# Kernel optimization log

Hardware: AMD Instinct MI355X
Metric: run time of the kernel (lower is better)

## Reference

```python
import jax, jax.numpy as jnp
import numpy as np

V, Tb, D, H, L = 50257, 1024, 768, 12, 12
HS = D // H  # head size 64
DF = 4 * D   # MLP hidden 3072


def setup_inputs() -> dict:
    key = jax.random.key(0)
    ks = jax.random.split(key, 24)
    s = 0.02
    inp = {}
    inp['x'] = jax.random.randint(ks[0], (1, Tb), 0, V, dtype=jnp.int64)
    inp['wte'] = jax.random.normal(ks[1], (V, D), jnp.float32) * s
    inp['wpe'] = jax.random.normal(ks[2], (Tb, D), jnp.float32) * s
    # per-layer, per-head QKV linears, stacked: [L, H, D, HS]
    inp['Wq'] = jax.random.normal(ks[3], (L, H, D, HS), jnp.float32) * s
    inp['bq'] = jnp.zeros((L, H, HS), jnp.float32)
    inp['Wk'] = jax.random.normal(ks[4], (L, H, D, HS), jnp.float32) * s
    inp['bk'] = jnp.zeros((L, H, HS), jnp.float32)
    inp['Wv'] = jax.random.normal(ks[5], (L, H, D, HS), jnp.float32) * s
    inp['bv'] = jnp.zeros((L, H, HS), jnp.float32)
    inp['ln1_s'] = jnp.ones((L, D), jnp.float32)
    inp['ln1_b'] = jnp.zeros((L, D), jnp.float32)
    inp['W1'] = jax.random.normal(ks[6], (L, D, DF), jnp.float32) * s
    inp['b1'] = jnp.zeros((L, DF), jnp.float32)
    inp['W2'] = jax.random.normal(ks[7], (L, DF, D), jnp.float32) * s
    inp['b2'] = jnp.zeros((L, D), jnp.float32)
    inp['ln2_s'] = jnp.ones((L, D), jnp.float32)
    inp['ln2_b'] = jnp.zeros((L, D), jnp.float32)
    inp['lnf_s'] = jnp.ones((D,), jnp.float32)
    inp['lnf_b'] = jnp.zeros((D,), jnp.float32)
    inp['Wlm'] = jax.random.normal(ks[8], (D, V), jnp.float32) * s
    return inp


def _layernorm(x, scale, bias, eps=1e-5):
    mu = jnp.mean(x, axis=-1, keepdims=True)
    var = jnp.var(x, axis=-1, keepdims=True)
    return (x - mu) * jax.lax.rsqrt(var + eps) * scale + bias


def _gpt2_forward(x, wte, wpe, Wq, bq, Wk, bk, Wv, bv, ln1_s, ln1_b,
                  W1, b1, W2, b2, ln2_s, ln2_b, lnf_s, lnf_b, Wlm):
    B, T = x.shape
    h = wte[x] + wpe[jnp.arange(T)][None]  # [B, T, D]
    mask = jnp.tril(jnp.ones((T, T), jnp.bool_))
    for l in range(L):
        xn = _layernorm(h, ln1_s[l], ln1_b[l])
        # per-head linears, stacked -> [B, H, T, HS]
        q = jnp.einsum('btd,hde->bhte', xn, Wq[l]) + bq[l][None, :, None, :]
        k = jnp.einsum('btd,hde->bhte', xn, Wk[l]) + bk[l][None, :, None, :]
        v = jnp.einsum('btd,hde->bhte', xn, Wv[l]) + bv[l][None, :, None, :]
        # NOTE: original module does NOT scale scores by 1/sqrt(head_size)
        scores = jnp.einsum('bhte,bhse->bhts', q, k)
        scores = jnp.where(mask[None, None], scores, -jnp.inf)
        w = jax.nn.softmax(scores, axis=-1)
        attn = jnp.einsum('bhts,bhse->bhte', w, v)
        attn = attn.transpose(0, 2, 1, 3).reshape(B, T, H * HS)
        h = h + attn  # residual (no output projection in original)
        xn2 = _layernorm(h, ln2_s[l], ln2_b[l])
        mlp = jnp.einsum('btd,df->btf', xn2, W1[l]) + b1[l]
        mlp = jax.nn.gelu(mlp, approximate=False)  # nn.GELU default = exact
        mlp = jnp.einsum('btf,fd->btd', mlp, W2[l]) + b2[l]
        h = h + mlp
    h = _layernorm(h, lnf_s, lnf_b)
    logits = jnp.einsum('btd,dv->btv', h, Wlm)  # lm_head, no bias
    return logits


def reference(x, wte, wpe, Wq, bq, Wk, bk, Wv, bv, ln1_s, ln1_b,
              W1, b1, W2, b2, ln2_s, ln2_b, lnf_s, lnf_b, Wlm):
    return _gpt2_forward(x, wte, wpe, Wq, bq, Wk, bk, Wv, bv, ln1_s, ln1_b,
                         W1, b1, W2, b2, ln2_s, ln2_b, lnf_s, lnf_b, Wlm)
```

## Files before the change

### kernel.cpp

```cpp
#include <hip/hip_runtime.h>
#include <math.h>

#define TLEN 1024
#define DM   768
#define NH   12
#define HSZ  64
#define DF_  3072
#define NL   12
#define VC   50257
#define VCP  50304
#define NPAN (VCP/128)

typedef __attribute__((ext_vector_type(8))) short bf16x8;
typedef __attribute__((ext_vector_type(4))) float f32x4;

__device__ __forceinline__ float gelu_exact(float x){
  return 0.5f * x * (1.0f + erff(x * 0.70710678118654752f));
}
__device__ __forceinline__ short f2bf(float f){
  union { float f; unsigned u; } x; x.f = f;
  unsigned r = x.u + 0x7fffu + ((x.u >> 16) & 1u);
  return (short)(r >> 16);
}
__device__ __forceinline__ void gl16(const void* g, void* l){
  __builtin_amdgcn_global_load_lds(
      (const __attribute__((address_space(1))) unsigned int*)g,
      (__attribute__((address_space(3))) unsigned int*)l, 16, 0, 0);
}

__global__ __launch_bounds__(256) void embedln_k(const int* __restrict__ x,
    const float* __restrict__ wte, const float* __restrict__ wpe,
    const float* __restrict__ sc, const float* __restrict__ bi,
    float* __restrict__ h, short* __restrict__ out)
{
  int w = threadIdx.x >> 6, lane = threadIdx.x & 63;
  int t = blockIdx.x * 4 + w;
  int tok = x[t];
  size_t off = (size_t)t * DM;
  float v[12];
  float s = 0.f, s2 = 0.f;
  #pragma unroll
  for (int i = 0; i < 12; i++){
    int c = lane + i * 64;
    float xv = wte[(size_t)tok * DM + c] + wpe[off + c];
    h[off + c] = xv;
    v[i] = xv; s += xv; s2 += xv * xv;
  }
  #pragma unroll
  for (int o = 32; o; o >>= 1){ s += __shfl_xor(s, o); s2 += __shfl_xor(s2, o); }
  float mu = s * (1.0f / DM);
  float var = s2 * (1.0f / DM) - mu * mu;
  float rs = rsqrtf(var + 1e-5f);
  #pragma unroll
  for (int i = 0; i < 12; i++){
    int c = lane + i * 64;
    out[off + c] = f2bf((v[i] - mu) * rs * sc[c] + bi[c]);
  }
}

__global__ __launch_bounds__(256) void ln_k(const float* __restrict__ in,
    const float* __restrict__ sc, const float* __restrict__ bi,
    short* __restrict__ out)
{
  int w = threadIdx.x >> 6, lane = threadIdx.x & 63;
  int row = blockIdx.x * 4 + w;
  const float* r = in + (size_t)row * DM;
  float v[12];
  float s = 0.f, s2 = 0.f;
  #pragma unroll
  for (int i = 0; i < 12; i++){
    float xv = r[lane + i * 64];
    v[i] = xv; s += xv; s2 += xv * xv;
  }
  #pragma unroll
  for (int o = 32; o; o >>= 1){ s += __shfl_xor(s, o); s2 += __shfl_xor(s2, o); }
  float mu  = s * (1.0f / DM);
  float var = s2 * (1.0f / DM) - mu * mu;
  float rs  = rsqrtf(var + 1e-5f);
  short* o = out + (size_t)row * DM;
  #pragma unroll
  for (int i = 0; i < 12; i++){
    int c = lane + i * 64;
    o[c] = f2bf((v[i] - mu) * rs * sc[c] + bi[c]);
  }
}

__global__ __launch_bounds__(256) void redln_k(float* __restrict__ h,
    const float* __restrict__ p0, const float* __restrict__ p1,
    const float* __restrict__ bias,
    const float* __restrict__ sc, const float* __restrict__ bi,
    short* __restrict__ out)
{
  int w = threadIdx.x >> 6, lane = threadIdx.x & 63;
  int row = blockIdx.x * 4 + w;
  size_t off = (size_t)row * DM;
  float v[12];
  float s = 0.f, s2 = 0.f;
  #pragma unroll
  for (int i = 0; i < 12; i++){
    int c = lane + i * 64;
    float xv = h[off + c] + p0[off + c] + p1[off + c] + bias[c];
    h[off + c] = xv;
    v[i] = xv; s += xv; s2 += xv * xv;
  }
  #pragma unroll
  for (int o = 32; o; o >>= 1){ s += __shfl_xor(s, o); s2 += __shfl_xor(s2, o); }
  float mu  = s * (1.0f / DM);
  float var = s2 * (1.0f / DM) - mu * mu;
  float rs  = rsqrtf(var + 1e-5f);
  #pragma unroll
  for (int i = 0; i < 12; i++){
    int c = lane + i * 64;
    out[off + c] = f2bf((v[i] - mu) * rs * sc[c] + bi[c]);
  }
}

__global__ __launch_bounds__(256) void tc_k(const float* __restrict__ in,
    short* __restrict__ out, int K, int N, int ntiles, int per_mat,
    size_t in_stride, size_t out_stride)
{
  __shared__ short sh[64][65];
  int b = blockIdx.x;
  int l = b / per_mat, r = b - l * per_mat;
  int nt = r % ntiles, kt = r / ntiles;
  const float* ip = in + (size_t)l * in_stride;
  short* op = out + (size_t)l * out_stride;
  int n0 = nt * 64, k0 = kt * 64;
  int tid = threadIdx.x;
  if ((N & 3) == 0){
    #pragma unroll
    for (int it = 0; it < 4; it++){
      int idx = it * 256 + tid;
      int k = idx >> 4, n4 = (idx & 15) * 4;
      float4 v = *(const float4*)(ip + (size_t)(k0 + k) * N + n0 + n4);
      sh[k][n4+0] = f2bf(v.x); sh[k][n4+1] = f2bf(v.y);
      sh[k][n4+2] = f2bf(v.z); sh[k][n4+3] = f2bf(v.w);
    }
  } else {
    #pragma unroll
    for (int it = 0; it < 16; it++){
      int idx = it * 256 + tid;
      int k = idx >> 6, n = idx & 63;
      float v = (n0 + n < N) ? ip[(size_t)(k0 + k) * N + n0 + n] : 0.f;
      sh[k][n] = f2bf(v);
    }
  }
  __syncthreads();
  #pragma unroll
  for (int it = 0; it < 2; it++){
    int n = it * 32 + (tid >> 3);
    int kc = (tid & 7) * 8;
    bf16x8 v;
    #pragma unroll
    for (int u = 0; u < 8; u++) v[u] = sh[kc + u][n];
    *(bf16x8*)(op + (size_t)(n0 + n) * K + k0 + kc) = v;
  }
}

__global__ __launch_bounds__(256) void tcqkv_k(const float* __restrict__ Wq,
    const float* __restrict__ Wk, const float* __restrict__ Wv,
    short* __restrict__ out)
{
  __shared__ short sh[64][65];
  int b = blockIdx.x;
  int l = b / 144; int r = b - l * 144;
  int h = r / 12, kt = r - h * 12;
  int tid = threadIdx.x;
  for (int p = 0; p < 3; p++){
    const float* ip = (p == 0 ? Wq : p == 1 ? Wk : Wv)
                      + ((size_t)(l * NH + h) * DM + kt * 64) * 64;
    if (p) __syncthreads();
    #pragma unroll
    for (int it = 0; it < 4; it++){
      int idx = it * 256 + tid;
      int k = idx >> 4, e4 = (idx & 15) * 4;
      float4 v = *(const float4*)(ip + (size_t)k * 64 + e4);
      sh[k][e4+0] = f2bf(v.x); sh[k][e4+1] = f2bf(v.y);
      sh[k][e4+2] = f2bf(v.z); sh[k][e4+3] = f2bf(v.w);
    }
    __syncthreads();
    short* op = out + (size_t)l * 2304 * DM + (size_t)(p * DM + h * 64) * DM;
    #pragma unroll
    for (int it = 0; it < 2; it++){
      int e = it * 32 + (tid >> 3);
      int kc = (tid & 7) * 8;
      bf16x8 v;
      #pragma unroll
      for (int u = 0; u < 8; u++) v[u] = sh[kc + u][e];
      *(bf16x8*)(op + (size_t)e * DM + kt * 64 + kc) = v;
    }
  }
}

template<int MODE, int FI, int FJ, int BK>
__global__ __launch_bounds__(256) void mg_k(
    const short* __restrict__ A, const short* __restrict__ Bt,
    const float* __restrict__ b0, const float* __restrict__ b1,
    const float* __restrict__ b2,
    void* __restrict__ C0, void* __restrict__ C1, void* __restrict__ C2)
{
  constexpr int LDA    = (MODE == 2) ? DF_ : DM;
  constexpr int BM     = FI * 32;
  constexpr int BN     = FJ * 32;
  constexpr int ABYTES = BM * BK * 2;
  constexpr int BBYTES = BN * BK * 2;
  constexpr int TBYTES = ABYTES + BBYTES;
  constexpr int DEPTH  = 2;
  constexpr int NBUF   = DEPTH + 1;
  constexpr int GR     = BK / 8;
  constexpr int NCHA   = ABYTES / 4096;
  constexpr int NCHB   = BBYTES / 4096;
  constexpr int W      = NCHA + NCHB;
  __shared__ __align__(16) char lds[NBUF * TBYTES];

  int tid = threadIdx.x;
  int wid = tid >> 6, lane = tid & 63;
  int l15 = lane & 15, l4 = lane >> 4;
  int wr = wid >> 1, wc = wid & 1;

  int m0, n0;
  if (MODE == 3){
    int xcd = blockIdx.x & 7, slot = blockIdx.x >> 3;
    int nb = xcd + 8 * (slot >> 3);
    if (nb >= NPAN) return;
    m0 = (slot & 7) * BM;
    n0 = nb * BN;
  } else {
    m0 = blockIdx.x * BM;
    n0 = blockIdx.y * BN;
  }
  int kbeg = (MODE == 2) ? blockIdx.z * (DF_ / 2) : 0;
  int nk   = ((MODE == 2) ? DF_ / 2 : LDA) / BK;

  f32x4 acc[FI][FJ] = {};
  int wbase = (tid & ~63) * 16;

  auto stage = [&](int k0, int b){
    char* ab = lds + b * TBYTES;
    char* bb = ab + ABYTES;
    #pragma unroll
    for (int ia = 0; ia < NCHA; ia++){
      int d = ia * 256 + tid;
      int row = d / GR, g = d & (GR - 1);
      int gs;
      if constexpr (BK == 64) gs = g ^ (row & 7);
      else                    gs = g ^ ((row >> 1) & 3);
      gl16(A + (size_t)(m0 + row) * LDA + k0 + gs * 8, ab + ia * 4096 + wbase);
    }
    #pragma unroll
    for (int ib = 0; ib < NCHB; ib++){
      int d = ib * 256 + tid;
      int row = d / GR, g = d & (GR - 1);
      int gs;
      if constexpr (BK == 64) gs = g ^ (row & 7);
      else                    gs = g ^ ((row >> 1) & 3);
      gl16(Bt + (size_t)(n0 + row) * LDA + k0 + gs * 8, bb + ib * 4096 + wbase);
    }
  };

  #pragma unroll
  for (int d = 0; d < DEPTH; d++)
    if (d < nk) stage(kbeg + d * BK, d);

  int cb = 0;
  int sb = DEPTH % NBUF;
  for (int t = 0; t < nk; ++t){
    if (t + DEPTH < nk){
      stage(kbeg + (t + DEPTH) * BK, sb);
      sb = (sb + 1 == NBUF) ? 0 : sb + 1;
      if constexpr (DEPTH * W == 4)       asm volatile("s_waitcnt vmcnt(4)"  ::: "memory");
      else if constexpr (DEPTH * W == 8)  asm volatile("s_waitcnt vmcnt(8)"  ::: "memory");
      else                                asm volatile("s_waitcnt vmcnt(16)" ::: "memory");
    } else if (DEPTH == 2 && t + 1 < nk){
      if constexpr (W == 4) asm volatile("s_waitcnt vmcnt(4)" ::: "memory");
      else                  asm volatile("s_waitcnt vmcnt(8)" ::: "memory");
    } else {
      asm volatile("s_waitcnt vmcnt(0)" ::: "memory");
    }
    __builtin_amdgcn_s_barrier();
    __builtin_amdgcn_sched_barrier(0);

    char* ab = lds + cb * TBYTES;
    char* bb = ab + ABYTES;
    cb = (cb + 1 == NBUF) ? 0 : cb + 1;
    #pragma unroll
    for (int kk = 0; kk < BK / 32; kk++){
      bf16x8 af[FI], bfr[FJ];
      #pragma unroll
      for (int i = 0; i < FI; i++){
        int row = wr * (FI * 16) + i * 16 + l15;
        int swz;
        if constexpr (BK == 64) swz = (kk * 4 + l4) ^ (row & 7);
        else                    swz = l4 ^ ((row >> 1) & 3);
        af[i] = *(const bf16x8*)(ab + row * (BK * 2) + swz * 16);
      }
      #pragma unroll
      for (int j = 0; j < FJ; j++){
        int row = wc * (FJ * 16) + j * 16 + l15;
        int swz;
        if constexpr (BK == 64) swz = (kk * 4 + l4) ^ (row & 7);
        else                    swz = l4 ^ ((row >> 1) & 3);
        bfr[j] = *(const bf16x8*)(bb + row * (BK * 2) + swz * 16);
      }
      #pragma unroll
      for (int i = 0; i < FI; i++)
        #pragma unroll
        for (int j = 0; j < FJ; j++)
          acc[i][j] = __builtin_amdgcn_mfma_f32_16x16x32_bf16(af[i], bfr[j], acc[i][j], 0, 0, 0);
    }
    __builtin_amdgcn_sched_barrier(0);
    __builtin_amdgcn_s_barrier();
  }

  #pragma unroll
  for (int i = 0; i < FI; i++){
    int rowb = m0 + wr * (FI * 16) + i * 16 + l4 * 4;
    #pragma unroll
    for (int j = 0; j < FJ; j++){
      int col = n0 + wc * (FJ * 16) + j * 16 + l15;
      if (MODE == 0){
        int p = col / DM, within = col - p * DM;
        const float* bp = (p == 0) ? b0 : (p == 1) ? b1 : b2;
        float bb2 = bp[within];
        int hd = within >> 6, e = within & 63;
        if (p < 2){
          short* dst = (short*)((p == 0) ? C0 : C1);
          #pragma unroll
          for (int r = 0; r < 4; r++)
            dst[((size_t)hd * TLEN + rowb + r) * 64 + e] = f2bf(acc[i][j][r] + bb2);
        } else {
          short4 pk;
          pk.x = f2bf(acc[i][j][0] + bb2); pk.y = f2bf(acc[i][j][1] + bb2);
          pk.z = f2bf(acc[i][j][2] + bb2); pk.w = f2bf(acc[i][j][3] + bb2);
          *(short4*)((short*)C2 + ((size_t)hd * 64 + e) * TLEN + rowb) = pk;
        }
      } else if (MODE == 1){
        #pragma unroll
        for (int r = 0; r < 4; r++)
          ((short*)C0)[(size_t)(rowb + r) * DF_ + col] =
              f2bf(gelu_exact(acc[i][j][r] + b0[col]));
      } else if (MODE == 2){
        float* dst = (float*)((blockIdx.z == 0) ? C0 : C1);
        #pragma unroll
        for (int r = 0; r < 4; r++)
          dst[(size_t)(rowb + r) * DM + col] = acc[i][j][r];
      } else {
        if (col < VC){
          #pragma unroll
          for (int r = 0; r < 4; r++)
            ((float*)C0)[(size_t)(rowb + r) * VC + col] = acc[i][j][r];
        }
      }
    }
  }
}

__global__ __launch_bounds__(256) void attn_k(const short* __restrict__ q,
    const short* __restrict__ k, const short* __restrict__ vt,
    float* __restrict__ h)
{
  __shared__ short P_lds[4][16][72];
  int tid = threadIdx.x;
  int wid = tid >> 6, lane = tid & 63;
  int l15 = lane & 15, l4 = lane >> 4;
  int head = blockIdx.x >> 4, qt = blockIdx.x & 15;
  int qb = qt * 64 + wid * 16;

  const short* qh = q  + (size_t)head * TLEN * 64;
  const short* kh = k  + (size_t)head * TLEN * 64;
  const short* vh = vt + (size_t)head * 64 * TLEN;

  bf16x8 qf[2];
  qf[0] = *(const bf16x8*)(qh + (size_t)(qb + l15) * 64 + l4 * 8);
  qf[1] = *(const bf16x8*)(qh + (size_t)(qb + l15) * 64 + 32 + l4 * 8);

  f32x4 O[4] = {};
  float mrow[4] = {-3e38f, -3e38f, -3e38f, -3e38f};
  float lrow[4] = {0.f, 0.f, 0.f, 0.f};

  for (int kv0 = 0; kv0 <= qb + 15; kv0 += 64){
    f32x4 S[4] = {};
    #pragma unroll
    for (int kk = 0; kk < 2; kk++){
      #pragma unroll
      for (int j = 0; j < 4; j++){
        bf16x8 kf = *(const bf16x8*)(kh + (size_t)(kv0 + j*16 + l15) * 64
                                     + kk*32 + l4*8);
        S[j] = __builtin_amdgcn_mfma_f32_16x16x32_bf16(qf[kk], kf, S[j], 0, 0, 0);
      }
    }
    if (kv0 + 63 > qb){
      #pragma unroll
      for (int j = 0; j < 4; j++){
        int kvc = kv0 + j*16 + l15;
        #pragma unroll
        for (int r = 0; r < 4; r++)
          if (kvc > qb + l4*4 + r) S[j][r] = -3e38f;
      }
    }
    #pragma unroll
    for (int r = 0; r < 4; r++){
      float mx = fmaxf(fmaxf(S[0][r], S[1][r]), fmaxf(S[2][r], S[3][r]));
      #pragma unroll
      for (int off = 1; off < 16; off <<= 1) mx = fmaxf(mx, __shfl_xor(mx, off));
      float mn = fmaxf(mrow[r], mx);
      float corr = __expf(mrow[r] - mn);
      mrow[r] = mn;
      float sm = 0.f;
      #pragma unroll
      for (int j = 0; j < 4; j++){
        float p = __expf(S[j][r] - mn);
        S[j][r] = p; sm += p;
      }
      #pragma unroll
      for (int off = 1; off < 16; off <<= 1) sm += __shfl_xor(sm, off);
      lrow[r] = lrow[r] * corr + sm;
      #pragma unroll
      for (int j = 0; j < 4; j++) O[j][r] *= corr;
    }
    #pragma unroll
    for (int j = 0; j < 4; j++)
      #pragma unroll
      for (int r = 0; r < 4; r++)
        P_lds[wid][l4*4 + r][j*16 + l15] = f2bf(S[j][r]);
    #pragma unroll
    for (int kk = 0; kk < 2; kk++){
      bf16x8 pa = *(const bf16x8*)(&P_lds[wid][l15][kk*32 + l4*8]);
      #pragma unroll
      for (int jd = 0; jd < 4; jd++){
        bf16x8 vf = *(const bf16x8*)(vh + (size_t)(jd*16 + l15) * TLEN
                                     + kv0 + kk*32 + l4*8);
        O[jd] = __builtin_amdgcn_mfma_f32_16x16x32_bf16(pa, vf, O[jd], 0, 0, 0);
      }
    }
  }

  #pragma unroll
  for (int r = 0; r < 4; r++){
    float inv = 1.0f / lrow[r];
    int t = qb + l4*4 + r;
    #pragma unroll
    for (int jd = 0; jd < 4; jd++){
      int d = head * 64 + jd*16 + l15;
      h[(size_t)t * DM + d] += O[jd][r] * inv;
    }
  }
}

extern "C" void kernel_launch(void* const* d_in, const int* in_sizes, int n_in,
                              void* d_out, int out_size, void* d_ws, size_t ws_size,
                              hipStream_t stream)
{
  const int*   x    = (const int*)  d_in[0];
  const float* wte  = (const float*)d_in[1];
  const float* wpe  = (const float*)d_in[2];
  const float* Wq   = (const float*)d_in[3];
  const float* bq   = (const float*)d_in[4];
  const float* Wk   = (const float*)d_in[5];
  const float* bk   = (const float*)d_in[6];
  const float* Wv   = (const float*)d_in[7];
  const float* bv   = (const float*)d_in[8];
  const float* ln1s = (const float*)d_in[9];
  const float* ln1b = (const float*)d_in[10];
  const float* W1   = (const float*)d_in[11];
  const float* b1   = (const float*)d_in[12];
  const float* W2   = (const float*)d_in[13];
  const float* b2   = (const float*)d_in[14];
  const float* ln2s = (const float*)d_in[15];
  const float* ln2b = (const float*)d_in[16];
  const float* lnfs = (const float*)d_in[17];
  const float* lnfb = (const float*)d_in[18];
  const float* Wlm  = (const float*)d_in[19];
  float* out = (float*)d_out;

  const size_t SZ_QKVT = (size_t)NL * 2304 * DM * 2;
  const size_t SZ_W1T  = (size_t)NL * DF_ * DM * 2;
  const size_t SZ_W2T  = (size_t)NL * DM * DF_ * 2;
  const size_t SZ_WLMT = (size_t)VCP * DM * 2;
  const size_t SZ_H    = (size_t)TLEN * DM * 4;
  const size_t SZ_BF   = (size_t)TLEN * DM * 2;

  char* ws = (char*)d_ws;
  short* wqkvT = (short*)ws;  ws += SZ_QKVT;
  short* w1T   = (short*)ws;  ws += SZ_W1T;
  short* w2T   = (short*)ws;  ws += SZ_W2T;
  short* wlmT  = (short*)ws;  ws += SZ_WLMT;
  float* h     = (float*)ws;  ws += SZ_H;
  short* qb    = (short*)ws;  ws += SZ_BF;
  short* kb    = (short*)ws;  ws += SZ_BF;
  short* vtb   = (short*)ws;  ws += SZ_BF;
  short* xnb   = (short*)ws;  ws += SZ_BF;
  short* mhb   = (short*)ws;  ws += (size_t)TLEN * DF_ * 2;
  float* p1    = (float*)ws;
  float* p0    = (float*)qb;

  tcqkv_k<<<NL*NH*12, 256, 0, stream>>>(Wq, Wk, Wv, wqkvT);
  tc_k<<<NL*48*12, 256, 0, stream>>>(W1, w1T, DM, DF_, 48, 576,
                                     (size_t)DM*DF_, (size_t)DM*DF_);
  tc_k<<<NL*12*48, 256, 0, stream>>>(W2, w2T, DF_, DM, 12, 576,
                                     (size_t)DM*DF_, (size_t)DM*DF_);
  tc_k<<<786*12, 256, 0, stream>>>(Wlm, wlmT, DM, VC, 786, 786*12, 0, 0);

  embedln_k<<<TLEN/4, 256, 0, stream>>>(x, wte, wpe, ln1s, ln1b, h, xnb);

  for (int l = 0; l < NL; ++l){
    mg_k<0,2,2,64><<<dim3(16,36), 256, 0, stream>>>(xnb, wqkvT + (size_t)l*2304*DM,
        bq + l*DM, bk + l*DM, bv + l*DM, qb, kb, vtb);
    attn_k<<<NH*16, 256, 0, stream>>>(qb, kb, vtb, h);
    ln_k<<<TLEN/4, 256, 0, stream>>>(h, ln2s + l*DM, ln2b + l*DM, xnb);
    mg_k<1,2,2,64><<<dim3(16,48), 256, 0, stream>>>(xnb, w1T + (size_t)l*DF_*DM,
        b1 + l*DF_, nullptr, nullptr, mhb, nullptr, nullptr);
    mg_k<2,2,2,64><<<dim3(16,12,2), 256, 0, stream>>>(mhb, w2T + (size_t)l*DM*DF_,
        nullptr, nullptr, nullptr, p0, p1, nullptr);
    const float* nsc = (l < NL-1) ? ln1s + (l+1)*DM : lnfs;
    const float* nbi = (l < NL-1) ? ln1b + (l+1)*DM : lnfb;
    redln_k<<<TLEN/4, 256, 0, stream>>>(h, p0, p1, b2 + l*DM, nsc, nbi, xnb);
  }

  mg_k<3,4,4,32><<<3200, 256, 0, stream>>>(xnb, wlmT,
      nullptr, nullptr, nullptr, out, nullptr, nullptr);
}
```

Baseline: 1.300 ms.

## Split attention KV range across waves with flash-decoding style LDS merge

Each block now handles one 16-row query tile per head, and its four waves split the causal KV steps among themselves instead of each wave owning a separate query tile. Partial max, sum and output accumulators are written to shared memory and wave 0 merges them with a log-sum-exp rescale before updating the residual. The grid grows from 192 to 768 blocks, which is meant to raise occupancy and balance the causal work better. The cost is extra shared memory, a block-wide barrier and a serial merge on one wave. Waves with an empty KV range still contribute neutral partials, since their stored max is very negative and their sums are zero.

```diff
diff --git a/kernel.cpp b/kernel.cpp
--- a/kernel.cpp
+++ b/kernel.cpp
@@ -360,11 +360,12 @@
     float* __restrict__ h)
 {
   __shared__ short P_lds[4][16][72];
+  __shared__ float M_lds[4][64][25];
   int tid = threadIdx.x;
   int wid = tid >> 6, lane = tid & 63;
   int l15 = lane & 15, l4 = lane >> 4;
-  int head = blockIdx.x >> 4, qt = blockIdx.x & 15;
-  int qb = qt * 64 + wid * 16;
+  int head = blockIdx.x >> 6, tile = blockIdx.x & 63;
+  int qb = tile * 16;
 
   const short* qh = q  + (size_t)head * TLEN * 64;
   const short* kh = k  + (size_t)head * TLEN * 64;
@@ -374,11 +375,17 @@
   qf[0] = *(const bf16x8*)(qh + (size_t)(qb + l15) * 64 + l4 * 8);
   qf[1] = *(const bf16x8*)(qh + (size_t)(qb + l15) * 64 + 32 + l4 * 8);
 
+  int nsteps = (qb + 15) / 64 + 1;
+  int spw = (nsteps + 3) >> 2;
+  int s_beg = wid * spw;
+  int s_end = s_beg + spw; if (s_end > nsteps) s_end = nsteps;
+
   f32x4 O[4] = {};
   float mrow[4] = {-3e38f, -3e38f, -3e38f, -3e38f};
   float lrow[4] = {0.f, 0.f, 0.f, 0.f};
 
-  for (int kv0 = 0; kv0 <= qb + 15; kv0 += 64){
+  for (int s = s_beg; s < s_end; ++s){
+    int kv0 = s * 64;
     f32x4 S[4] = {};
     #pragma unroll
     for (int kk = 0; kk < 2; kk++){
@@ -437,12 +444,45 @@
 
   #pragma unroll
   for (int r = 0; r < 4; r++){
-    float inv = 1.0f / lrow[r];
-    int t = qb + l4*4 + r;
-    #pragma unroll
-    for (int jd = 0; jd < 4; jd++){
-      int d = head * 64 + jd*16 + l15;
-      h[(size_t)t * DM + d] += O[jd][r] * inv;
+    M_lds[wid][lane][r]     = mrow[r];
+    M_lds[wid][lane][4 + r] = lrow[r];
+  }
+  #pragma unroll
+  for (int jd = 0; jd < 4; jd++)
+    #pragma unroll
+    for (int r = 0; r < 4; r++)
+      M_lds[wid][lane][8 + jd*4 + r] = O[jd][r];
+  __syncthreads();
+
+  if (wid == 0){
+    float Mt[4], Lt[4];
+    f32x4 Ot[4] = {};
+    #pragma unroll
+    for (int r = 0; r < 4; r++){
+      Mt[r] = fmaxf(fmaxf(M_lds[0][lane][r], M_lds[1][lane][r]),
+                    fmaxf(M_lds[2][lane][r], M_lds[3][lane][r]));
+      Lt[r] = 0.f;
+    }
+    #pragma unroll
+    for (int w = 0; w < 4; w++){
+      #pragma unroll
+      for (int r = 0; r < 4; r++){
+        float c = __expf(M_lds[w][lane][r] - Mt[r]);
+        Lt[r] += M_lds[w][lane][4 + r] * c;
+        #pragma unroll
+        for (int jd = 0; jd < 4; jd++)
+          Ot[jd][r] += M_lds[w][lane][8 + jd*4 + r] * c;
+      }
+    }
+    #pragma unroll
+    for (int r = 0; r < 4; r++){
+      float inv = 1.0f / Lt[r];
+      int t = qb + l4*4 + r;
+      #pragma unroll
+      for (int jd = 0; jd < 4; jd++){
+        int d = head * 64 + jd*16 + l15;
+        h[(size_t)t * DM + d] += Ot[jd][r] * inv;
+      }
     }
   }
 }
@@ -506,7 +546,7 @@
   for (int l = 0; l < NL; ++l){
     mg_k<0,2,2,64><<<dim3(16,36), 256, 0, stream>>>(xnb, wqkvT + (size_t)l*2304*DM,
         bq + l*DM, bk + l*DM, bv + l*DM, qb, kb, vtb);
-    attn_k<<<NH*16, 256, 0, stream>>>(qb, kb, vtb, h);
+    attn_k<<<NH*64, 256, 0, stream>>>(qb, kb, vtb, h);
     ln_k<<<TLEN/4, 256, 0, stream>>>(h, ln2s + l*DM, ln2b + l*DM, xnb);
     mg_k<1,2,2,64><<<dim3(16,48), 256, 0, stream>>>(xnb, w1T + (size_t)l*DF_*DM,
         b1 + l*DF_, nullptr, nullptr, mhb, nullptr, nullptr);
```

New measurement: 1.222 ms. 1.06x faster.
